# Kernel optimization log

Hardware: AMD Instinct MI355X
Metric: run time of the kernel (lower is better)

## Reference

```python
import jax, jax.numpy as jnp
import numpy as np

B, C_IN, C_OUT, H, W, K = 64, 64, 64, 64, 64, 3
MEM_DECAY, MEM_RESET = 0.99, 0.1
TH_DECAY, TH_RESET = 0.95, 1.0
TR_DECAY = 0.95
A_POS, A_NEG = 0.005, 0.005
W_CLIP = 0.1


def _conv(x, w, groups=1):
    # cross-correlation, stride 1, padding 1 (matches F.conv2d(..., padding=1))
    return jax.lax.conv_general_dilated(
        x, w, window_strides=(1, 1), padding=((1, 1), (1, 1)),
        dimension_numbers=('NCHW', 'OIHW', 'NCHW'), feature_group_count=groups)


def setup_inputs() -> dict:
    key = jax.random.key(0)
    k1, k2 = jax.random.split(key)
    in_spikes = (jax.random.uniform(k1, (B, C_IN, H, W)) < 0.1).astype(jnp.float32)
    weights = jax.random.normal(k2, (C_OUT, C_IN, K, K), jnp.float32) * (1.0 / (C_IN * K * K))
    membrane = jnp.full((B, C_OUT, H, W), MEM_RESET, jnp.float32)
    thresholds = jnp.full((B, C_OUT, H, W), TH_RESET, jnp.float32)
    trace_pre = jnp.ones((B, C_IN, H, W), jnp.float32)
    trace_post = jnp.ones((B, C_OUT, H, W), jnp.float32)
    return {"in_spikes": in_spikes, "weights": weights, "membrane": membrane,
            "thresholds": thresholds, "trace_pre": trace_pre, "trace_post": trace_post}


def reference(in_spikes, weights, membrane, thresholds, trace_pre, trace_post):
    # LIF dynamics
    mem_pot = _conv(in_spikes, weights)                      # (B, C_OUT, H, W)
    mem = membrane * MEM_DECAY + mem_pot
    spikes = (mem > thresholds).astype(mem.dtype)
    fired = spikes > 0
    new_mem = jnp.where(fired, MEM_RESET, mem)
    new_th = jnp.where(fired, TH_RESET, thresholds * TH_DECAY)
    # STDP traces (train=True path)
    new_pre = jnp.clip(trace_pre * TR_DECAY + in_spikes, 0.0, 1.0)
    new_post = jnp.clip(trace_post * TR_DECAY + spikes, 0.0, 1.0)
    # per-out-channel full-window correlation (original python loop over channels,
    # here a single grouped conv): kernel = batch-mean trace of that channel
    avg_pre = jnp.mean(new_pre[:, :C_OUT], axis=0)           # (C_OUT, H, W)
    avg_post = jnp.mean(new_post, axis=0)                    # (C_OUT, H, W)
    pot = _conv(new_post, (A_POS * avg_pre)[:, None], groups=C_OUT)   # (B, C_OUT, 3, 3)
    dep = _conv(new_post, (A_NEG * avg_post)[:, None], groups=C_OUT)  # (B, C_OUT, 3, 3)
    delta = jnp.mean(pot - dep, axis=0)                      # (C_OUT, 3, 3)
    new_w = jnp.clip(weights + jnp.broadcast_to(delta[:, None], weights.shape), -W_CLIP, W_CLIP)
    return spikes, new_mem, new_th, new_pre, new_post, new_w
```

## Files before the change

### kernel.cpp

```cpp
#include <hip/hip_runtime.h>

typedef __attribute__((ext_vector_type(8))) short bf16x8;
typedef __attribute__((ext_vector_type(16))) float f32x16;

namespace {
constexpr int BB   = 64;
constexpr int CC   = 64;
constexpr int HH   = 64;
constexpr int WW   = 64;
constexpr int HW   = HH * WW;
constexpr int CHW  = CC * HW;
constexpr int NTOT = BB * CHW;
}

__device__ __forceinline__ ushort f2bf(float f) {
    union { float f; unsigned u; } x; x.f = f;
    unsigned r = x.u + 0x7fffu + ((x.u >> 16) & 1u);
    return (ushort)(r >> 16);
}

__device__ __forceinline__ f32x16 zero16() {
    f32x16 z;
#pragma unroll
    for (int i = 0; i < 16; ++i) z[i] = 0.f;
    return z;
}

__global__ void k_prep_w(const float* __restrict__ w, ushort* __restrict__ wimg)
{
    const int e = blockIdx.x * 256 + threadIdx.x;
    if (e >= 36864) return;
    const int ci07 = e & 7;
    const int co   = (e >> 3) & 63;
    const int gidx = e >> 9;
    const int gp   = gidx & 1;
    const int s    = (gidx >> 1) % 12;
    const int dx   = gidx / 24;
    const int dy   = s >> 2;
    const int ci   = (s & 3) * 16 + gp * 8 + ci07;
    wimg[e] = f2bf(w[((co * 64 + ci) * 3 + dy) * 3 + dx]);
}

__global__ __launch_bounds__(256, 2) void k_conv_lif(
    const float* __restrict__ xin, const ushort* __restrict__ wimg,
    const float* __restrict__ membrane, const float* __restrict__ thresh,
    const float* __restrict__ tpre, const float* __restrict__ tpost,
    float* __restrict__ o_spk, float* __restrict__ o_mem, float* __restrict__ o_th,
    float* __restrict__ o_pre, float* __restrict__ o_post)
{
    __shared__ __align__(16) short in_lds[6 * 66 * 64];
    __shared__ __align__(16) short w_lds[1536 * 8];

    const int tid = threadIdx.x;
    const int b   = blockIdx.x >> 4;
    const int y0  = (blockIdx.x & 15) << 2;

    for (int it = tid; it < 3168; it += 256) {
        const int n  = it % 66;
        const int t2 = it / 66;
        const int g  = t2 & 7;
        const int r  = t2 >> 3;
        const int gx = n - 1;
        const int gy = y0 + r - 1;
        const bool inb = ((unsigned)gx < 64u) && ((unsigned)gy < 64u);
        const int base = ((b * 64 + g * 8) * 64 + gy) * 64 + gx;
        float v[8];
#pragma unroll
        for (int j = 0; j < 8; ++j) {
            float f = 0.f;
            if (inb) f = xin[base + j * 4096];
            v[j] = f;
        }
        bf16x8 hv;
#pragma unroll
        for (int j = 0; j < 8; ++j) hv[j] = (short)f2bf(v[j]);
        *(bf16x8*)&in_lds[(r * 66 + n) * 64 + ((g ^ (n & 7)) << 3)] = hv;
        if (r >= 1 && r <= 4 && inb) {
#pragma unroll
            for (int j = 0; j < 8; ++j) {
                const float q = tpre[base + j * 4096] * 0.95f + v[j];
                o_pre[base + j * 4096] = fminf(fmaxf(q, 0.f), 1.f);
            }
        }
    }
    for (int i = tid; i < 1536; i += 256)
        *(bf16x8*)&w_lds[i * 8] = *(const bf16x8*)&wimg[i * 8];
    __syncthreads();

    const int wv = tid >> 6, ln = tid & 63;
    const int ch = wv >> 1, xh = wv & 1;
    const int lh = ln >> 5, l5 = ln & 31;

    f32x16 acc0 = zero16(), acc1 = zero16(), acc2 = zero16(), acc3 = zero16();

    for (int dx = 0; dx < 3; ++dx) {
        if (dx) {
            __syncthreads();
            for (int i = tid; i < 1536; i += 256)
                *(bf16x8*)&w_lds[i * 8] = *(const bf16x8*)&wimg[dx * 12288 + i * 8];
            __syncthreads();
        }
        const int nsl = xh * 32 + l5 + dx;
        const int n7  = nsl & 7;
#pragma unroll
        for (int s = 0; s < 12; ++s) {
            const bf16x8 a = *(const bf16x8*)&w_lds[(((s * 2 + lh) * 64) + ch * 32 + l5) * 8];
            const int dy   = s >> 2;
            const int gsw  = (2 * (s & 3) + lh) ^ n7;
            const int boff = (dy * 66 + nsl) * 64 + (gsw << 3);
            acc0 = __builtin_amdgcn_mfma_f32_32x32x16_bf16(
                       a, *(const bf16x8*)&in_lds[boff           ], acc0, 0, 0, 0);
            acc1 = __builtin_amdgcn_mfma_f32_32x32x16_bf16(
                       a, *(const bf16x8*)&in_lds[boff + 1*66*64], acc1, 0, 0, 0);
            acc2 = __builtin_amdgcn_mfma_f32_32x32x16_bf16(
                       a, *(const bf16x8*)&in_lds[boff + 2*66*64], acc2, 0, 0, 0);
            acc3 = __builtin_amdgcn_mfma_f32_32x32x16_bf16(
                       a, *(const bf16x8*)&in_lds[boff + 3*66*64], acc3, 0, 0, 0);
        }
    }

    const int x = xh * 32 + l5;
#define EPILOG(ACC, Y)                                                          \
    {                                                                           \
        const int gy = y0 + (Y);                                                \
        _Pragma("unroll")                                                       \
        for (int rr = 0; rr < 16; ++rr) {                                       \
            const int co  = ch * 32 + (rr & 3) + 8 * (rr >> 2) + 4 * lh;        \
            const int idx = ((b * 64 + co) * 64 + gy) * 64 + x;                 \
            const float mem = membrane[idx] * 0.99f + (ACC)[rr];                \
            const float tv  = thresh[idx];                                      \
            const float sp  = (mem > tv) ? 1.f : 0.f;                           \
            o_spk[idx] = sp;                                                    \
            o_mem[idx] = (sp > 0.f) ? 0.1f : mem;                               \
            o_th[idx]  = (sp > 0.f) ? 1.0f : tv * 0.95f;                        \
            const float q = tpost[idx] * 0.95f + sp;                            \
            o_post[idx] = fminf(fmaxf(q, 0.f), 1.f);                            \
        }                                                                       \
    }
    EPILOG(acc0, 0)
    EPILOG(acc1, 1)
    EPILOG(acc2, 2)
    EPILOG(acc3, 3)
#undef EPILOG
}

__global__ void k_avg(const float4* __restrict__ pre, const float4* __restrict__ post,
                      float4* __restrict__ apre, float4* __restrict__ apost)
{
    const int i = blockIdx.x * 256 + threadIdx.x;
    float4 s1 = make_float4(0.f, 0.f, 0.f, 0.f);
    float4 s2 = make_float4(0.f, 0.f, 0.f, 0.f);
    for (int bb = 0; bb < BB; ++bb) {
        const float4 p = pre[bb * (CHW / 4) + i];
        const float4 q = post[bb * (CHW / 4) + i];
        s1.x += p.x; s1.y += p.y; s1.z += p.z; s1.w += p.w;
        s2.x += q.x; s2.y += q.y; s2.z += q.z; s2.w += q.w;
    }
    const float sc = 1.f / 64.f;
    apre[i]  = make_float4(s1.x * sc, s1.y * sc, s1.z * sc, s1.w * sc);
    apost[i] = make_float4(s2.x * sc, s2.y * sc, s2.z * sc, s2.w * sc);
}

__global__ __launch_bounds__(256) void k_wupd(const float* __restrict__ avg_pre,
                                              const float* __restrict__ avg_post,
                                              const float* __restrict__ wgt,
                                              float* __restrict__ o_w)
{
    __shared__ float sp[4096];
    __shared__ float sq[66 * 66];
    __shared__ float sacc[18];
    __shared__ float sdelta[9];
    const int c = blockIdx.x, tid = threadIdx.x;

    for (int t = tid; t < 66 * 66; t += 256) sq[t] = 0.f;
    if (tid < 18) sacc[tid] = 0.f;
    __syncthreads();
    for (int t = tid; t < 4096; t += 256) {
        sp[t] = avg_pre[c * HW + t];
        sq[((t >> 6) + 1) * 66 + (t & 63) + 1] = avg_post[c * HW + t];
    }
    __syncthreads();

    float pot[9] = {0,0,0,0,0,0,0,0,0};
    float dep[9] = {0,0,0,0,0,0,0,0,0};
    for (int t = tid; t < 4096; t += 256) {
        const int yy = t >> 6, xx = t & 63;
        const float p = sp[t];
        const float q = sq[(yy + 1) * 66 + xx + 1];
#pragma unroll
        for (int dy = 0; dy < 3; ++dy)
#pragma unroll
            for (int dxx = 0; dxx < 3; ++dxx) {
                const float v = sq[(yy + dy) * 66 + xx + dxx];
                pot[dy * 3 + dxx] += v * p;
                dep[dy * 3 + dxx] += v * q;
            }
    }
#pragma unroll
    for (int k = 0; k < 18; ++k) {
        float v = (k < 9) ? pot[k] : dep[k - 9];
        for (int off = 32; off > 0; off >>= 1) v += __shfl_down(v, off, 64);
        if ((tid & 63) == 0) atomicAdd(&sacc[k], v);
    }
    __syncthreads();
    if (tid < 9) sdelta[tid] = 0.005f * sacc[tid] - 0.005f * sacc[tid + 9];
    __syncthreads();
    for (int t = tid; t < 576; t += 256) {
        const float v = wgt[c * 576 + t] + sdelta[t % 9];
        o_w[c * 576 + t] = fminf(fmaxf(v, -0.1f), 0.1f);
    }
}

extern "C" void kernel_launch(void* const* d_in, const int* in_sizes, int n_in,
                              void* d_out, int out_size, void* d_ws, size_t ws_size,
                              hipStream_t stream)
{
    const float* xin   = (const float*)d_in[0];
    const float* wgt   = (const float*)d_in[1];
    const float* mem   = (const float*)d_in[2];
    const float* th    = (const float*)d_in[3];
    const float* tpre  = (const float*)d_in[4];
    const float* tpost = (const float*)d_in[5];

    float* out    = (float*)d_out;
    float* o_spk  = out;
    float* o_mem  = out + (size_t)1 * NTOT;
    float* o_th   = out + (size_t)2 * NTOT;
    float* o_pre  = out + (size_t)3 * NTOT;
    float* o_post = out + (size_t)4 * NTOT;
    float* o_w    = out + (size_t)5 * NTOT;

    ushort* wimg    = (ushort*)d_ws;
    float* avg_pre  = (float*)((char*)d_ws + 73728);
    float* avg_post = avg_pre + CHW;

    hipLaunchKernelGGL(k_prep_w, dim3(144), dim3(256), 0, stream, wgt, wimg);
    hipLaunchKernelGGL(k_conv_lif, dim3(1024), dim3(256), 0, stream,
                       xin, wimg, mem, th, tpre, tpost,
                       o_spk, o_mem, o_th, o_pre, o_post);
    hipLaunchKernelGGL(k_avg, dim3(256), dim3(256), 0, stream,
                       (const float4*)o_pre, (const float4*)o_post,
                       (float4*)avg_pre, (float4*)avg_post);
    hipLaunchKernelGGL(k_wupd, dim3(64), dim3(256), 0, stream,
                       avg_pre, avg_post, wgt, o_w);
}
```

Before: 615.9 us.

## Fuse batch-mean trace reduction into conv kernel via atomics, drop weight LDS staging

Removes the separate k_avg pass, which re-read both pre and post trace outputs. Batch averages are now accumulated with float atomicAdd directly in the conv/LIF kernel, after a new zeroing kernel. Weights are read straight from global/L2 instead of being staged in LDS, which also removes the per-dx barriers. Occupancy is raised to three blocks per SIMD. This trades a 128 MB re-read for about 33M contended atomics, and makes the float sum order nondeterministic.

```diff
diff --git a/kernel.cpp b/kernel.cpp
--- a/kernel.cpp
+++ b/kernel.cpp
@@ -41,15 +41,20 @@
     wimg[e] = f2bf(w[((co * 64 + ci) * 3 + dy) * 3 + dx]);
 }
 
-__global__ __launch_bounds__(256, 2) void k_conv_lif(
+__global__ void k_zero(float4* __restrict__ p)
+{
+    p[blockIdx.x * 256 + threadIdx.x] = make_float4(0.f, 0.f, 0.f, 0.f);
+}
+
+__global__ __launch_bounds__(256, 3) void k_conv_lif(
     const float* __restrict__ xin, const ushort* __restrict__ wimg,
     const float* __restrict__ membrane, const float* __restrict__ thresh,
     const float* __restrict__ tpre, const float* __restrict__ tpost,
     float* __restrict__ o_spk, float* __restrict__ o_mem, float* __restrict__ o_th,
-    float* __restrict__ o_pre, float* __restrict__ o_post)
+    float* __restrict__ o_pre, float* __restrict__ o_post,
+    float* __restrict__ avg_pre, float* __restrict__ avg_post)
 {
     __shared__ __align__(16) short in_lds[6 * 66 * 64];
-    __shared__ __align__(16) short w_lds[1536 * 8];
 
     const int tid = threadIdx.x;
     const int b   = blockIdx.x >> 4;
@@ -76,15 +81,16 @@
         for (int j = 0; j < 8; ++j) hv[j] = (short)f2bf(v[j]);
         *(bf16x8*)&in_lds[(r * 66 + n) * 64 + ((g ^ (n & 7)) << 3)] = hv;
         if (r >= 1 && r <= 4 && inb) {
+            const int cbase = ((g * 8) * 64 + gy) * 64 + gx;
 #pragma unroll
             for (int j = 0; j < 8; ++j) {
-                const float q = tpre[base + j * 4096] * 0.95f + v[j];
-                o_pre[base + j * 4096] = fminf(fmaxf(q, 0.f), 1.f);
+                const float q  = tpre[base + j * 4096] * 0.95f + v[j];
+                const float qc = fminf(fmaxf(q, 0.f), 1.f);
+                o_pre[base + j * 4096] = qc;
+                atomicAdd(&avg_pre[cbase + j * 4096], qc * (1.f / 64.f));
             }
         }
     }
-    for (int i = tid; i < 1536; i += 256)
-        *(bf16x8*)&w_lds[i * 8] = *(const bf16x8*)&wimg[i * 8];
     __syncthreads();
 
     const int wv = tid >> 6, ln = tid & 63;
@@ -94,17 +100,12 @@
     f32x16 acc0 = zero16(), acc1 = zero16(), acc2 = zero16(), acc3 = zero16();
 
     for (int dx = 0; dx < 3; ++dx) {
-        if (dx) {
-            __syncthreads();
-            for (int i = tid; i < 1536; i += 256)
-                *(bf16x8*)&w_lds[i * 8] = *(const bf16x8*)&wimg[dx * 12288 + i * 8];
-            __syncthreads();
-        }
+        const ushort* wp = wimg + dx * 12288;
         const int nsl = xh * 32 + l5 + dx;
         const int n7  = nsl & 7;
 #pragma unroll
         for (int s = 0; s < 12; ++s) {
-            const bf16x8 a = *(const bf16x8*)&w_lds[(((s * 2 + lh) * 64) + ch * 32 + l5) * 8];
+            const bf16x8 a = *(const bf16x8*)&wp[(((s * 2 + lh) << 6) + (ch << 5) + l5) * 8];
             const int dy   = s >> 2;
             const int gsw  = (2 * (s & 3) + lh) ^ n7;
             const int boff = (dy * 66 + nsl) * 64 + (gsw << 3);
@@ -133,8 +134,10 @@
             o_spk[idx] = sp;                                                    \
             o_mem[idx] = (sp > 0.f) ? 0.1f : mem;                               \
             o_th[idx]  = (sp > 0.f) ? 1.0f : tv * 0.95f;                        \
-            const float q = tpost[idx] * 0.95f + sp;                            \
-            o_post[idx] = fminf(fmaxf(q, 0.f), 1.f);                            \
+            const float q  = tpost[idx] * 0.95f + sp;                           \
+            const float qc = fminf(fmaxf(q, 0.f), 1.f);                         \
+            o_post[idx] = qc;                                                   \
+            atomicAdd(&avg_post[(co * 64 + gy) * 64 + x], qc * (1.f / 64.f));   \
         }                                                                       \
     }
     EPILOG(acc0, 0)
@@ -142,23 +145,6 @@
     EPILOG(acc2, 2)
     EPILOG(acc3, 3)
 #undef EPILOG
-}
-
-__global__ void k_avg(const float4* __restrict__ pre, const float4* __restrict__ post,
-                      float4* __restrict__ apre, float4* __restrict__ apost)
-{
-    const int i = blockIdx.x * 256 + threadIdx.x;
-    float4 s1 = make_float4(0.f, 0.f, 0.f, 0.f);
-    float4 s2 = make_float4(0.f, 0.f, 0.f, 0.f);
-    for (int bb = 0; bb < BB; ++bb) {
-        const float4 p = pre[bb * (CHW / 4) + i];
-        const float4 q = post[bb * (CHW / 4) + i];
-        s1.x += p.x; s1.y += p.y; s1.z += p.z; s1.w += p.w;
-        s2.x += q.x; s2.y += q.y; s2.z += q.z; s2.w += q.w;
-    }
-    const float sc = 1.f / 64.f;
-    apre[i]  = make_float4(s1.x * sc, s1.y * sc, s1.z * sc, s1.w * sc);
-    apost[i] = make_float4(s2.x * sc, s2.y * sc, s2.z * sc, s2.w * sc);
 }
 
 __global__ __launch_bounds__(256) void k_wupd(const float* __restrict__ avg_pre,
@@ -235,12 +221,10 @@
     float* avg_post = avg_pre + CHW;
 
     hipLaunchKernelGGL(k_prep_w, dim3(144), dim3(256), 0, stream, wgt, wimg);
+    hipLaunchKernelGGL(k_zero, dim3(512), dim3(256), 0, stream, (float4*)avg_pre);
     hipLaunchKernelGGL(k_conv_lif, dim3(1024), dim3(256), 0, stream,
                        xin, wimg, mem, th, tpre, tpost,
-                       o_spk, o_mem, o_th, o_pre, o_post);
-    hipLaunchKernelGGL(k_avg, dim3(256), dim3(256), 0, stream,
-                       (const float4*)o_pre, (const float4*)o_post,
-                       (float4*)avg_pre, (float4*)avg_post);
+                       o_spk, o_mem, o_th, o_pre, o_post, avg_pre, avg_post);
     hipLaunchKernelGGL(k_wupd, dim3(64), dim3(256), 0, stream,
                        avg_pre, avg_post, wgt, o_w);
 }
```

Result: slower. 750.7 us (+21.9%).
